# Optimization experiments

Hardware: AMD Instinct MI355X
Metric: run time of the kernel (lower is better)

## Reference

```python
import jax, jax.numpy as jnp
import numpy as np

NUM_NODES = 50000
NUM_CLASSES = 10


def gcn_conv(x, W, b, src, dst, num_nodes):
    """PyG GCNConv: add self-loops, symmetric D^-1/2 (A+I) D^-1/2 normalization."""
    h = x @ W  # [N, C_out]
    # degree with self-loops: count of incoming edges per node + 1
    deg = jax.ops.segment_sum(jnp.ones_like(dst, dtype=h.dtype), dst,
                              num_segments=num_nodes) + 1.0
    dinv = jax.lax.rsqrt(deg)  # [N]
    norm_e = dinv[src] * dinv[dst]  # [E] edge norm
    msg = h[src] * norm_e[:, None]  # [E, C_out] gathered messages
    agg = jax.ops.segment_sum(msg, dst, num_segments=num_nodes)
    # self-loop contribution: norm = deg_i^-1
    agg = agg + h * (1.0 / deg)[:, None]
    return agg + b


def setup_inputs() -> dict:
    key = jax.random.key(0)
    ks = jax.random.split(key, 8)
    C_in, C_hid, C_out = 128, 128, 128
    E = 800000
    x = jax.random.normal(ks[0], (NUM_NODES, C_in), dtype=jnp.float32)
    edge_index = jax.random.randint(ks[1], (2, E), 0, NUM_NODES, dtype=jnp.int64)
    s1 = 1.0 / np.sqrt(C_in)
    s2 = 1.0 / np.sqrt(C_hid)
    s3 = 1.0 / np.sqrt(C_out)
    W1 = jax.random.uniform(ks[2], (C_in, C_hid), jnp.float32, -s1, s1)
    b1 = jnp.zeros((C_hid,), jnp.float32)
    W2 = jax.random.uniform(ks[3], (C_hid, C_out), jnp.float32, -s2, s2)
    b2 = jnp.zeros((C_out,), jnp.float32)
    Wl = jax.random.uniform(ks[4], (C_out, NUM_CLASSES), jnp.float32, -s3, s3)
    bl = jax.random.uniform(ks[5], (NUM_CLASSES,), jnp.float32, -s3, s3)
    return {"x": x, "edge_index": edge_index, "W1": W1, "b1": b1,
            "W2": W2, "b2": b2, "Wl": Wl, "bl": bl}


def reference(x, edge_index, W1, b1, W2, b2, Wl, bl):
    src, dst = edge_index[0], edge_index[1]
    h = gcn_conv(x, W1, b1, src, dst, NUM_NODES)
    h = jax.nn.relu(h)
    h = gcn_conv(h, W2, b2, src, dst, NUM_NODES)
    h = jax.nn.relu(h)
    return h @ Wl + bl
```

## Files before the change

### kernel.cpp

```cpp
#include <hip/hip_runtime.h>
#include <hip/hip_fp16.h>

#define C 128

typedef _Float16 half8 __attribute__((ext_vector_type(8)));
typedef float f32x4 __attribute__((ext_vector_type(4)));

__global__ __launch_bounds__(256) void k_zero(int* __restrict__ cnt, int N) {
    int i = blockIdx.x * 256 + threadIdx.x;
    if (i < N) cnt[i] = 0;
}

__global__ __launch_bounds__(256) void k_histr(const int* __restrict__ dst,
                                               int* __restrict__ cnt,
                                               unsigned short* __restrict__ rank,
                                               int E) {
    int e = blockIdx.x * 256 + threadIdx.x;
    if (e < E) rank[e] = (unsigned short)atomicAdd(&cnt[dst[e]], 1);
}

__global__ __launch_bounds__(256) void k_scan1(const int* __restrict__ cnt,
                                               int* __restrict__ partials, int N) {
    __shared__ int sdata[256];
    int i = blockIdx.x * 256 + threadIdx.x;
    sdata[threadIdx.x] = (i < N) ? cnt[i] : 0;
    __syncthreads();
    for (int s = 128; s > 0; s >>= 1) {
        if (threadIdx.x < s) sdata[threadIdx.x] += sdata[threadIdx.x + s];
        __syncthreads();
    }
    if (threadIdx.x == 0) partials[blockIdx.x] = sdata[0];
}

__global__ __launch_bounds__(256) void k_scan2(int* __restrict__ partials, int nb) {
    __shared__ int s[2][256];
    int t = threadIdx.x;
    if (nb <= 256) {
        int v = (t < nb) ? partials[t] : 0;
        int buf = 0;
        s[0][t] = v;
        __syncthreads();
        for (int off = 1; off < 256; off <<= 1) {
            int x = s[buf][t];
            if (t >= off) x += s[buf][t - off];
            s[buf ^ 1][t] = x;
            buf ^= 1;
            __syncthreads();
        }
        if (t < nb) partials[t] = s[buf][t] - v;
    } else if (t == 0) {
        int run = 0;
        for (int b = 0; b < nb; ++b) { int v = partials[b]; partials[b] = run; run += v; }
    }
}

__global__ __launch_bounds__(256) void k_scan3(const int* __restrict__ cnt,
                                               const int* __restrict__ partials,
                                               int* __restrict__ rowptr,
                                               float* __restrict__ dinv,
                                               int N, int E) {
    __shared__ int s[2][256];
    int i = blockIdx.x * 256 + threadIdx.x;
    int v = (i < N) ? cnt[i] : 0;
    int buf = 0;
    s[0][threadIdx.x] = v;
    __syncthreads();
    for (int off = 1; off < 256; off <<= 1) {
        int t = s[buf][threadIdx.x];
        if (threadIdx.x >= off) t += s[buf][threadIdx.x - off];
        s[buf ^ 1][threadIdx.x] = t;
        buf ^= 1;
        __syncthreads();
    }
    int incl = s[buf][threadIdx.x];
    int excl = incl - v + partials[blockIdx.x];
    if (i < N) {
        rowptr[i] = excl;
        dinv[i] = rsqrtf((float)v + 1.0f);
    }
    if (i == 0) rowptr[N] = E;
}

__global__ __launch_bounds__(256) void k_fill2(const int* __restrict__ src,
                                               const int* __restrict__ dst,
                                               const unsigned short* __restrict__ rank,
                                               const int* __restrict__ rowptr,
                                               unsigned short* __restrict__ col, int E) {
    int e = blockIdx.x * 256 + threadIdx.x;
    if (e >= E) return;
    int pos = rowptr[dst[e]] + (int)rank[e];
    col[pos] = (unsigned short)src[e];
}

__global__ __launch_bounds__(256) void k_gemm_mfma(const float* __restrict__ X,
                                                   const float* __restrict__ W,
                                                   const float* __restrict__ dinv,
                                                   _Float16* __restrict__ Hs16,
                                                   int M) {
    __shared__ _Float16 WtH[C * C];
    __shared__ _Float16 WtL[C * C];
    const int t = threadIdx.x;

    for (int idx = t; idx < C * C; idx += 256) {
        int k = idx >> 7, n = idx & 127;
        float w = W[idx];
        _Float16 h = (_Float16)w;
        _Float16 l = (_Float16)(w - (float)h);
        int off = n * C + (((k >> 3) ^ (n & 15)) << 3) + (k & 7);
        WtH[off] = h;
        WtL[off] = l;
    }
    __syncthreads();

    const int wv = t >> 6, lane = t & 63;
    const int l15 = lane & 15, lg = lane >> 4;
    const int rowA = blockIdx.x * 64 + wv * 16 + l15;
    const bool aok = rowA < M;
    const float* xrow = X + (size_t)rowA * C;

    f32x4 acc[8];
#pragma unroll
    for (int i = 0; i < 8; ++i) acc[i] = (f32x4){0.f, 0.f, 0.f, 0.f};

#pragma unroll
    for (int ks = 0; ks < 4; ++ks) {
        const int k0 = ks * 32 + lg * 8;
        float4 x0 = make_float4(0.f, 0.f, 0.f, 0.f);
        float4 x1 = make_float4(0.f, 0.f, 0.f, 0.f);
        if (aok) {
            x0 = *(const float4*)(xrow + k0);
            x1 = *(const float4*)(xrow + k0 + 4);
        }
        half8 ah, al;
        {
            _Float16 h;
            h = (_Float16)x0.x; ah[0] = h; al[0] = (_Float16)(x0.x - (float)h);
            h = (_Float16)x0.y; ah[1] = h; al[1] = (_Float16)(x0.y - (float)h);
            h = (_Float16)x0.z; ah[2] = h; al[2] = (_Float16)(x0.z - (float)h);
            h = (_Float16)x0.w; ah[3] = h; al[3] = (_Float16)(x0.w - (float)h);
            h = (_Float16)x1.x; ah[4] = h; al[4] = (_Float16)(x1.x - (float)h);
            h = (_Float16)x1.y; ah[5] = h; al[5] = (_Float16)(x1.y - (float)h);
            h = (_Float16)x1.z; ah[6] = h; al[6] = (_Float16)(x1.z - (float)h);
            h = (_Float16)x1.w; ah[7] = h; al[7] = (_Float16)(x1.w - (float)h);
        }
        const int chb = ks * 4 + lg;
#pragma unroll
        for (int ct = 0; ct < 8; ++ct) {
            const int n = ct * 16 + l15;
            const int off = n * C + ((chb ^ l15) << 3);
            half8 bh = *(const half8*)&WtH[off];
            half8 bl = *(const half8*)&WtL[off];
            acc[ct] = __builtin_amdgcn_mfma_f32_16x16x32_f16(ah, bh, acc[ct], 0, 0, 0);
            acc[ct] = __builtin_amdgcn_mfma_f32_16x16x32_f16(al, bh, acc[ct], 0, 0, 0);
            acc[ct] = __builtin_amdgcn_mfma_f32_16x16x32_f16(ah, bl, acc[ct], 0, 0, 0);
        }
    }

    const int rowC = blockIdx.x * 64 + wv * 16 + lg * 4;
#pragma unroll
    for (int r = 0; r < 4; ++r) {
        int row = rowC + r;
        if (row >= M) continue;
        float s = dinv[row];
#pragma unroll
        for (int ct = 0; ct < 8; ++ct) {
            Hs16[(size_t)row * C + ct * 16 + l15] = (_Float16)(acc[ct][r] * s);
        }
    }
}

__global__ __launch_bounds__(256) void k_aggf(const _Float16* __restrict__ Hs16,
                                              const int* __restrict__ rowptr,
                                              const unsigned short* __restrict__ col,
                                              const float* __restrict__ dinv,
                                              const float* __restrict__ b,
                                              float* __restrict__ Out, int N) {
    const int node = blockIdx.x * 8 + (threadIdx.x >> 5);
    const int lane = threadIdx.x & 31;
    if (node >= N) return;
    const uint2* __restrict__ H16 = (const uint2*)Hs16;

    uint2 qs = H16[(size_t)node * 32 + lane];
    float2 sa = __half22float2(*(__half2*)&qs.x);
    float2 sb = __half22float2(*(__half2*)&qs.y);
    float4 acc = make_float4(sa.x, sa.y, sb.x, sb.y);

    const int e0 = rowptr[node], e1 = rowptr[node + 1];
    int j = e0;
    for (; j + 4 <= e1; j += 4) {
        int n0 = col[j + 0], n1 = col[j + 1], n2 = col[j + 2], n3 = col[j + 3];
        uint2 q0 = H16[(size_t)n0 * 32 + lane];
        uint2 q1 = H16[(size_t)n1 * 32 + lane];
        uint2 q2 = H16[(size_t)n2 * 32 + lane];
        uint2 q3 = H16[(size_t)n3 * 32 + lane];
        float2 a0 = __half22float2(*(__half2*)&q0.x), b0 = __half22float2(*(__half2*)&q0.y);
        float2 a1 = __half22float2(*(__half2*)&q1.x), b1_ = __half22float2(*(__half2*)&q1.y);
        float2 a2 = __half22float2(*(__half2*)&q2.x), b2_ = __half22float2(*(__half2*)&q2.y);
        float2 a3 = __half22float2(*(__half2*)&q3.x), b3_ = __half22float2(*(__half2*)&q3.y);
        acc.x += (a0.x + a1.x) + (a2.x + a3.x);
        acc.y += (a0.y + a1.y) + (a2.y + a3.y);
        acc.z += (b0.x + b1_.x) + (b2_.x + b3_.x);
        acc.w += (b0.y + b1_.y) + (b2_.y + b3_.y);
    }
    for (; j < e1; ++j) {
        int n = col[j];
        uint2 q = H16[(size_t)n * 32 + lane];
        float2 a = __half22float2(*(__half2*)&q.x);
        float2 c = __half22float2(*(__half2*)&q.y);
        acc.x += a.x; acc.y += a.y; acc.z += c.x; acc.w += c.y;
    }
    const float s = dinv[node];
    const float4 bb = *(const float4*)(b + lane * 4);
    float4 o;
    o.x = s * acc.x + bb.x; o.y = s * acc.y + bb.y;
    o.z = s * acc.z + bb.z; o.w = s * acc.w + bb.w;
    o.x = o.x > 0.f ? o.x : 0.f;
    o.y = o.y > 0.f ? o.y : 0.f;
    o.z = o.z > 0.f ? o.z : 0.f;
    o.w = o.w > 0.f ? o.w : 0.f;
    ((float4*)Out)[(size_t)node * 32 + lane] = o;
}

__global__ __launch_bounds__(256) void k_final(const float* __restrict__ H,
                                               const float* __restrict__ Wl,
                                               const float* __restrict__ bl,
                                               float* __restrict__ out, int M) {
    __shared__ float wl[C * 10];
    __shared__ float bls[16];
    for (int i = threadIdx.x; i < C * 10; i += 256) wl[i] = Wl[i];
    if (threadIdx.x < 10) bls[threadIdx.x] = bl[threadIdx.x];
    __syncthreads();

    long long g = (long long)blockIdx.x * 256 + threadIdx.x;
    int i = (int)(g >> 4);
    int j = (int)(g & 15);
    if (i >= M || j >= 10) return;
    const float4* h4 = (const float4*)(H + (size_t)i * C);
    float acc = bls[j];
#pragma unroll 8
    for (int c4 = 0; c4 < 32; ++c4) {
        float4 hv = h4[c4];
        int cb = c4 * 4;
        acc += hv.x * wl[(cb + 0) * 10 + j] + hv.y * wl[(cb + 1) * 10 + j] +
               hv.z * wl[(cb + 2) * 10 + j] + hv.w * wl[(cb + 3) * 10 + j];
    }
    out[(size_t)i * 10 + j] = acc;
}

extern "C" void kernel_launch(void* const* d_in, const int* in_sizes, int n_in,
                              void* d_out, int out_size, void* d_ws, size_t ws_size,
                              hipStream_t stream) {
    const float* x  = (const float*)d_in[0];
    const int*   ei = (const int*)d_in[1];
    const float* W1 = (const float*)d_in[2];
    const float* b1 = (const float*)d_in[3];
    const float* W2 = (const float*)d_in[4];
    const float* b2 = (const float*)d_in[5];
    const float* Wl = (const float*)d_in[6];
    const float* bl = (const float*)d_in[7];
    float* out = (float*)d_out;

    const int N = in_sizes[0] / C;
    const int E = in_sizes[1] / 2;
    const int* src = ei;
    const int* dst = ei + E;

    char* p = (char*)d_ws;
    _Float16* bufHs16 = (_Float16*)p;  p += (size_t)N * C * 2;
    float*    bufT    = (float*)p;     p += (size_t)N * C * 4;
    int*      cnt     = (int*)p;       p += (size_t)N * 4;
    int*      rowptr  = (int*)p;       p += (size_t)(N + 1) * 4;
    float*    dinv    = (float*)p;     p += (size_t)N * 4;
    int*      partials= (int*)p;       p += 1024;
    unsigned short* rank   = (unsigned short*)p;  p += (size_t)E * 2;
    unsigned short* colidx = (unsigned short*)p;

    const int gridN   = (N + 255) / 256;
    const int gridE   = (E + 255) / 256;
    const int gridGemm = (N + 63) / 64;
    const int gridAgg = (N + 7) / 8;
    const int gridFin = (int)(((long long)N * 16 + 255) / 256);

    k_zero<<<gridN, 256, 0, stream>>>(cnt, N);
    k_histr<<<gridE, 256, 0, stream>>>(dst, cnt, rank, E);
    k_scan1<<<gridN, 256, 0, stream>>>(cnt, partials, N);
    k_scan2<<<1, 256, 0, stream>>>(partials, gridN);
    k_scan3<<<gridN, 256, 0, stream>>>(cnt, partials, rowptr, dinv, N, E);
    k_fill2<<<gridE, 256, 0, stream>>>(src, dst, rank, rowptr, colidx, E);

    k_gemm_mfma<<<gridGemm, 256, 0, stream>>>(x, W1, dinv, bufHs16, N);
    k_aggf<<<gridAgg, 256, 0, stream>>>(bufHs16, rowptr, colidx, dinv, b1, bufT, N);

    k_gemm_mfma<<<gridGemm, 256, 0, stream>>>(bufT, W2, dinv, bufHs16, N);
    k_aggf<<<gridAgg, 256, 0, stream>>>(bufHs16, rowptr, colidx, dinv, b2, bufT, N);

    k_final<<<gridFin, 256, 0, stream>>>(bufT, Wl, bl, out, N);
}
```

Baseline: 266.7 us.

## Sort nodes by degree, store layer-1 output in fp16, fuse final linear

```diff
diff --git a/kernel.cpp b/kernel.cpp
--- a/kernel.cpp
+++ b/kernel.cpp
@@ -1,14 +1,17 @@
 #include <hip/hip_runtime.h>
 #include <hip/hip_fp16.h>
+#include <type_traits>
 
 #define C 128
 
 typedef _Float16 half8 __attribute__((ext_vector_type(8)));
 typedef float f32x4 __attribute__((ext_vector_type(4)));
 
-__global__ __launch_bounds__(256) void k_zero(int* __restrict__ cnt, int N) {
+__global__ __launch_bounds__(256) void k_zero(int* __restrict__ cnt,
+                                              int* __restrict__ degbins, int N) {
     int i = blockIdx.x * 256 + threadIdx.x;
     if (i < N) cnt[i] = 0;
+    if (i < 256) degbins[i] = 0;
 }
 
 __global__ __launch_bounds__(256) void k_histr(const int* __restrict__ dst,
@@ -58,6 +61,7 @@
                                                const int* __restrict__ partials,
                                                int* __restrict__ rowptr,
                                                float* __restrict__ dinv,
+                                               int* __restrict__ degbins,
                                                int N, int E) {
     __shared__ int s[2][256];
     int i = blockIdx.x * 256 + threadIdx.x;
@@ -77,8 +81,41 @@
     if (i < N) {
         rowptr[i] = excl;
         dinv[i] = rsqrtf((float)v + 1.0f);
+        int b = v > 255 ? 255 : v;
+        atomicAdd(&degbins[b], 1);
     }
     if (i == 0) rowptr[N] = E;
+}
+
+__global__ __launch_bounds__(256) void k_degscan(int* __restrict__ degbins,
+                                                 int* __restrict__ degfill) {
+    __shared__ int s[2][256];
+    int t = threadIdx.x;
+    int v = degbins[t];
+    int buf = 0;
+    s[0][t] = v;
+    __syncthreads();
+    for (int off = 1; off < 256; off <<= 1) {
+        int x = s[buf][t];
+        if (t >= off) x += s[buf][t - off];
+        s[buf ^ 1][t] = x;
+        buf ^= 1;
+        __syncthreads();
+    }
+    degbins[t] = s[buf][t] - v;
+    degfill[t] = 0;
+}
+
+__global__ __launch_bounds__(256) void k_permfill(const int* __restrict__ cnt,
+                                                  const int* __restrict__ degbins,
+                                                  int* __restrict__ degfill,
+                                                  int* __restrict__ perm, int N) {
+    int i = blockIdx.x * 256 + threadIdx.x;
+    if (i >= N) return;
+    int d = cnt[i];
+    d = d > 255 ? 255 : d;
+    int pos = degbins[d] + atomicAdd(&degfill[d], 1);
+    perm[pos] = i;
 }
 
 __global__ __launch_bounds__(256) void k_fill2(const int* __restrict__ src,
@@ -92,7 +129,8 @@
     col[pos] = (unsigned short)src[e];
 }
 
-__global__ __launch_bounds__(256) void k_gemm_mfma(const float* __restrict__ X,
+template <typename TA>
+__global__ __launch_bounds__(256) void k_gemm_mfma(const TA* __restrict__ X,
                                                    const float* __restrict__ W,
                                                    const float* __restrict__ dinv,
                                                    _Float16* __restrict__ Hs16,
@@ -116,7 +154,7 @@
     const int l15 = lane & 15, lg = lane >> 4;
     const int rowA = blockIdx.x * 64 + wv * 16 + l15;
     const bool aok = rowA < M;
-    const float* xrow = X + (size_t)rowA * C;
+    const TA* xrow = X + (size_t)rowA * C;
 
     f32x4 acc[8];
 #pragma unroll
@@ -125,23 +163,24 @@
 #pragma unroll
     for (int ks = 0; ks < 4; ++ks) {
         const int k0 = ks * 32 + lg * 8;
-        float4 x0 = make_float4(0.f, 0.f, 0.f, 0.f);
-        float4 x1 = make_float4(0.f, 0.f, 0.f, 0.f);
-        if (aok) {
-            x0 = *(const float4*)(xrow + k0);
-            x1 = *(const float4*)(xrow + k0 + 4);
-        }
-        half8 ah, al;
-        {
-            _Float16 h;
-            h = (_Float16)x0.x; ah[0] = h; al[0] = (_Float16)(x0.x - (float)h);
-            h = (_Float16)x0.y; ah[1] = h; al[1] = (_Float16)(x0.y - (float)h);
-            h = (_Float16)x0.z; ah[2] = h; al[2] = (_Float16)(x0.z - (float)h);
-            h = (_Float16)x0.w; ah[3] = h; al[3] = (_Float16)(x0.w - (float)h);
-            h = (_Float16)x1.x; ah[4] = h; al[4] = (_Float16)(x1.x - (float)h);
-            h = (_Float16)x1.y; ah[5] = h; al[5] = (_Float16)(x1.y - (float)h);
-            h = (_Float16)x1.z; ah[6] = h; al[6] = (_Float16)(x1.z - (float)h);
-            h = (_Float16)x1.w; ah[7] = h; al[7] = (_Float16)(x1.w - (float)h);
+        half8 ah = (half8)(_Float16)0;
+        half8 al = (half8)(_Float16)0;
+        if constexpr (std::is_same_v<TA, float>) {
+            if (aok) {
+                float4 x0 = *(const float4*)(xrow + k0);
+                float4 x1 = *(const float4*)(xrow + k0 + 4);
+                _Float16 h;
+                h = (_Float16)x0.x; ah[0] = h; al[0] = (_Float16)(x0.x - (float)h);
+                h = (_Float16)x0.y; ah[1] = h; al[1] = (_Float16)(x0.y - (float)h);
+                h = (_Float16)x0.z; ah[2] = h; al[2] = (_Float16)(x0.z - (float)h);
+                h = (_Float16)x0.w; ah[3] = h; al[3] = (_Float16)(x0.w - (float)h);
+                h = (_Float16)x1.x; ah[4] = h; al[4] = (_Float16)(x1.x - (float)h);
+                h = (_Float16)x1.y; ah[5] = h; al[5] = (_Float16)(x1.y - (float)h);
+                h = (_Float16)x1.z; ah[6] = h; al[6] = (_Float16)(x1.z - (float)h);
+                h = (_Float16)x1.w; ah[7] = h; al[7] = (_Float16)(x1.w - (float)h);
+            }
+        } else {
+            if (aok) ah = *(const half8*)(xrow + k0);
         }
         const int chb = ks * 4 + lg;
 #pragma unroll
@@ -151,7 +190,8 @@
             half8 bh = *(const half8*)&WtH[off];
             half8 bl = *(const half8*)&WtL[off];
             acc[ct] = __builtin_amdgcn_mfma_f32_16x16x32_f16(ah, bh, acc[ct], 0, 0, 0);
-            acc[ct] = __builtin_amdgcn_mfma_f32_16x16x32_f16(al, bh, acc[ct], 0, 0, 0);
+            if constexpr (std::is_same_v<TA, float>)
+                acc[ct] = __builtin_amdgcn_mfma_f32_16x16x32_f16(al, bh, acc[ct], 0, 0, 0);
             acc[ct] = __builtin_amdgcn_mfma_f32_16x16x32_f16(ah, bl, acc[ct], 0, 0, 0);
         }
     }
@@ -169,15 +209,26 @@
     }
 }
 
+template <int MODE>
 __global__ __launch_bounds__(256) void k_aggf(const _Float16* __restrict__ Hs16,
                                               const int* __restrict__ rowptr,
                                               const unsigned short* __restrict__ col,
+                                              const int* __restrict__ perm,
                                               const float* __restrict__ dinv,
                                               const float* __restrict__ b,
-                                              float* __restrict__ Out, int N) {
-    const int node = blockIdx.x * 8 + (threadIdx.x >> 5);
+                                              const float* __restrict__ Wl,
+                                              const float* __restrict__ bl,
+                                              void* __restrict__ OutP, int N) {
+    __shared__ float wlds[(MODE == 1) ? C * 10 : 1];
+    if (MODE == 1) {
+        for (int i = threadIdx.x; i < C * 10; i += 256) wlds[i] = Wl[i];
+        __syncthreads();
+    }
+
+    const int gid = blockIdx.x * 8 + (threadIdx.x >> 5);
     const int lane = threadIdx.x & 31;
-    if (node >= N) return;
+    if (gid >= N) return;
+    const int node = perm[gid];
     const uint2* __restrict__ H16 = (const uint2*)Hs16;
 
     uint2 qs = H16[(size_t)node * 32 + lane];
@@ -187,20 +238,33 @@
 
     const int e0 = rowptr[node], e1 = rowptr[node + 1];
     int j = e0;
+    for (; j + 8 <= e1; j += 8) {
+        uint2 q[8];
+#pragma unroll
+        for (int u = 0; u < 8; ++u) {
+            int n = col[j + u];
+            q[u] = H16[(size_t)n * 32 + lane];
+        }
+#pragma unroll
+        for (int u = 0; u < 8; ++u) {
+            float2 a = __half22float2(*(__half2*)&q[u].x);
+            float2 c = __half22float2(*(__half2*)&q[u].y);
+            acc.x += a.x; acc.y += a.y; acc.z += c.x; acc.w += c.y;
+        }
+    }
     for (; j + 4 <= e1; j += 4) {
-        int n0 = col[j + 0], n1 = col[j + 1], n2 = col[j + 2], n3 = col[j + 3];
-        uint2 q0 = H16[(size_t)n0 * 32 + lane];
-        uint2 q1 = H16[(size_t)n1 * 32 + lane];
-        uint2 q2 = H16[(size_t)n2 * 32 + lane];
-        uint2 q3 = H16[(size_t)n3 * 32 + lane];
-        float2 a0 = __half22float2(*(__half2*)&q0.x), b0 = __half22float2(*(__half2*)&q0.y);
-        float2 a1 = __half22float2(*(__half2*)&q1.x), b1_ = __half22float2(*(__half2*)&q1.y);
-        float2 a2 = __half22float2(*(__half2*)&q2.x), b2_ = __half22float2(*(__half2*)&q2.y);
-        float2 a3 = __half22float2(*(__half2*)&q3.x), b3_ = __half22float2(*(__half2*)&q3.y);
-        acc.x += (a0.x + a1.x) + (a2.x + a3.x);
-        acc.y += (a0.y + a1.y) + (a2.y + a3.y);
-        acc.z += (b0.x + b1_.x) + (b2_.x + b3_.x);
-        acc.w += (b0.y + b1_.y) + (b2_.y + b3_.y);
+        uint2 q[4];
+#pragma unroll
+        for (int u = 0; u < 4; ++u) {
+            int n = col[j + u];
+            q[u] = H16[(size_t)n * 32 + lane];
+        }
+#pragma unroll
+        for (int u = 0; u < 4; ++u) {
+            float2 a = __half22float2(*(__half2*)&q[u].x);
+            float2 c = __half22float2(*(__half2*)&q[u].y);
+            acc.x += a.x; acc.y += a.y; acc.z += c.x; acc.w += c.y;
+        }
     }
     for (; j < e1; ++j) {
         int n = col[j];
@@ -209,6 +273,7 @@
         float2 c = __half22float2(*(__half2*)&q.y);
         acc.x += a.x; acc.y += a.y; acc.z += c.x; acc.w += c.y;
     }
+
     const float s = dinv[node];
     const float4 bb = *(const float4*)(b + lane * 4);
     float4 o;
@@ -218,33 +283,38 @@
     o.y = o.y > 0.f ? o.y : 0.f;
     o.z = o.z > 0.f ? o.z : 0.f;
     o.w = o.w > 0.f ? o.w : 0.f;
-    ((float4*)Out)[(size_t)node * 32 + lane] = o;
-}
-
-__global__ __launch_bounds__(256) void k_final(const float* __restrict__ H,
-                                               const float* __restrict__ Wl,
-                                               const float* __restrict__ bl,
-                                               float* __restrict__ out, int M) {
-    __shared__ float wl[C * 10];
-    __shared__ float bls[16];
-    for (int i = threadIdx.x; i < C * 10; i += 256) wl[i] = Wl[i];
-    if (threadIdx.x < 10) bls[threadIdx.x] = bl[threadIdx.x];
-    __syncthreads();
-
-    long long g = (long long)blockIdx.x * 256 + threadIdx.x;
-    int i = (int)(g >> 4);
-    int j = (int)(g & 15);
-    if (i >= M || j >= 10) return;
-    const float4* h4 = (const float4*)(H + (size_t)i * C);
-    float acc = bls[j];
-#pragma unroll 8
-    for (int c4 = 0; c4 < 32; ++c4) {
-        float4 hv = h4[c4];
-        int cb = c4 * 4;
-        acc += hv.x * wl[(cb + 0) * 10 + j] + hv.y * wl[(cb + 1) * 10 + j] +
-               hv.z * wl[(cb + 2) * 10 + j] + hv.w * wl[(cb + 3) * 10 + j];
-    }
-    out[(size_t)i * 10 + j] = acc;
+
+    if (MODE == 0) {
+        __half2 h01 = __floats2half2_rn(o.x, o.y);
+        __half2 h23 = __floats2half2_rn(o.z, o.w);
+        uint2 pk;
+        pk.x = *(unsigned int*)&h01;
+        pk.y = *(unsigned int*)&h23;
+        ((uint2*)OutP)[(size_t)node * 32 + lane] = pk;
+    } else {
+        float p[10];
+        const int c0 = lane * 4;
+#pragma unroll
+        for (int k = 0; k < 10; ++k) {
+            p[k] = o.x * wlds[(c0 + 0) * 10 + k] + o.y * wlds[(c0 + 1) * 10 + k] +
+                   o.z * wlds[(c0 + 2) * 10 + k] + o.w * wlds[(c0 + 3) * 10 + k];
+        }
+#pragma unroll
+        for (int k = 0; k < 10; ++k) {
+            float v = p[k];
+            v += __shfl_xor(v, 1);
+            v += __shfl_xor(v, 2);
+            v += __shfl_xor(v, 4);
+            v += __shfl_xor(v, 8);
+            v += __shfl_xor(v, 16);
+            p[k] = v;
+        }
+        if (lane == 0) {
+            float* outp = (float*)OutP + (size_t)node * 10;
+#pragma unroll
+            for (int k = 0; k < 10; ++k) outp[k] = p[k] + bl[k];
+        }
+    }
 }
 
 extern "C" void kernel_launch(void* const* d_in, const int* in_sizes, int n_in,
@@ -267,11 +337,14 @@
 
     char* p = (char*)d_ws;
     _Float16* bufHs16 = (_Float16*)p;  p += (size_t)N * C * 2;
-    float*    bufT    = (float*)p;     p += (size_t)N * C * 4;
+    _Float16* bufT16  = (_Float16*)p;  p += (size_t)N * C * 2;
     int*      cnt     = (int*)p;       p += (size_t)N * 4;
     int*      rowptr  = (int*)p;       p += (size_t)(N + 1) * 4;
     float*    dinv    = (float*)p;     p += (size_t)N * 4;
+    int*      perm    = (int*)p;       p += (size_t)N * 4;
     int*      partials= (int*)p;       p += 1024;
+    int*      degbins = (int*)p;       p += 1024;
+    int*      degfill = (int*)p;       p += 1024;
     unsigned short* rank   = (unsigned short*)p;  p += (size_t)E * 2;
     unsigned short* colidx = (unsigned short*)p;
 
@@ -279,20 +352,21 @@
     const int gridE   = (E + 255) / 256;
     const int gridGemm = (N + 63) / 64;
     const int gridAgg = (N + 7) / 8;
-    const int gridFin = (int)(((long long)N * 16 + 255) / 256);
-
-    k_zero<<<gridN, 256, 0, stream>>>(cnt, N);
+
+    k_zero<<<gridN, 256, 0, stream>>>(cnt, degbins, N);
     k_histr<<<gridE, 256, 0, stream>>>(dst, cnt, rank, E);
     k_scan1<<<gridN, 256, 0, stream>>>(cnt, partials, N);
     k_scan2<<<1, 256, 0, stream>>>(partials, gridN);
-    k_scan3<<<gridN, 256, 0, stream>>>(cnt, partials, rowptr, dinv, N, E);
+    k_scan3<<<gridN, 256, 0, stream>>>(cnt, partials, rowptr, dinv, degbins, N, E);
+    k_degscan<<<1, 256, 0, stream>>>(degbins, degfill);
+    k_permfill<<<gridN, 256, 0, stream>>>(cnt, degbins, degfill, perm, N);
     k_fill2<<<gridE, 256, 0, stream>>>(src, dst, rank, rowptr, colidx, E);
 
-    k_gemm_mfma<<<gridGemm, 256, 0, stream>>>(x, W1, dinv, bufHs16, N);
-    k_aggf<<<gridAgg, 256, 0, stream>>>(bufHs16, rowptr, colidx, dinv, b1, bufT, N);
-
-    k_gemm_mfma<<<gridGemm, 256, 0, stream>>>(bufT, W2, dinv, bufHs16, N);
-    k_aggf<<<gridAgg, 256, 0, stream>>>(bufHs16, rowptr, colidx, dinv, b2, bufT, N);
-
-    k_final<<<gridFin, 256, 0, stream>>>(bufT, Wl, bl, out, N);
-}
+    k_gemm_mfma<float><<<gridGemm, 256, 0, stream>>>(x, W1, dinv, bufHs16, N);
+    k_aggf<0><<<gridAgg, 256, 0, stream>>>(bufHs16, rowptr, colidx, perm, dinv,
+                                           b1, nullptr, nullptr, bufT16, N);
+
+    k_gemm_mfma<_Float16><<<gridGemm, 256, 0, stream>>>(bufT16, W2, dinv, bufHs16, N);
+    k_aggf<1><<<gridAgg, 256, 0, stream>>>(bufHs16, rowptr, colidx, perm, dinv,
+                                           b2, Wl, bl, out, N);
+}
```

Result: slower. 532.6 us (+99.7%).
